# Kernel tuning notes

Measured on AMD Instinct MI355X. Metric: run time of the kernel, lower is better.

The kernel has to match this reference:

```python
import jax, jax.numpy as jnp
import numpy as np

MARGIN = 0.3
EPS = 1e-8  # torch CosineSimilarity eps

N, D = 16384, 256


def setup_inputs() -> dict:
    key = jax.random.key(0)
    k1, k2 = jax.random.split(key)
    x = jax.random.normal(k1, (N, D), dtype=jnp.float32)
    y = jax.random.normal(k2, (N, D), dtype=jnp.float32)
    return {"x": x, "y": y}


def _cosine_matrix(x, y):
    # torch cosine_similarity: dot / max(|x||y|, eps). Normalize rows with eps clamp.
    xn = x / jnp.maximum(jnp.linalg.norm(x, axis=-1, keepdims=True), EPS)
    yn = y / jnp.maximum(jnp.linalg.norm(y, axis=-1, keepdims=True), EPS)
    return xn @ yn.T  # [N, N]


def _rank(S):
    # S[i, j] = cos(x_i, y_j). Positive pair on diagonal.
    diag = jnp.diagonal(S)                      # [N]
    E = jnp.exp(S)                              # [N, N]
    neg_sum = jnp.sum(E, axis=1) - jnp.exp(diag)  # sum over n != i of exp(cos(x_i, y_n))
    m = jnp.exp(diag - MARGIN)                  # margin only on positive term
    ret = m / (m + neg_sum)
    return -jnp.mean(ret)


def reference(x, y):
    S = _cosine_matrix(x, y)
    # bidirectional: rank(x, y) + rank(y, x); rank(y, x) uses transposed sims
    return _rank(S) + _rank(S.T)
```

## Files before the change

### kernel.cpp

```cpp
#include <hip/hip_runtime.h>

#define N_ROWS 16384
#define DIM 256
#define MARGINF 0.3f
#define CH 1024
#define NT 64
#define LOG2E 1.44269504089f

typedef float f32x4 __attribute__((ext_vector_type(4)));
typedef int i32x4 __attribute__((ext_vector_type(4)));
typedef int i32x8 __attribute__((ext_vector_type(8)));

__device__ __forceinline__ float fexp2(float x) {
#if __has_builtin(__builtin_amdgcn_exp2f)
  return __builtin_amdgcn_exp2f(x);
#else
  return exp2f(x);
#endif
}

__device__ __forceinline__ unsigned char to_e4m3(float f) {
  unsigned u = __float_as_uint(f);
  unsigned sign = (u >> 24) & 0x80u;
  float a = fabsf(f);
  if (a >= 448.0f) return (unsigned char)(sign | 0x7eu);
  if (a < 0.015625f) {
    int q = (int)(a * 512.0f + 0.5f);
    return (unsigned char)(sign | (unsigned)q);
  }
  int e;
  float m = frexpf(a, &e);
  float mant = 2.0f * m;
  int e8 = e - 1;
  int mb = (int)(mant * 8.0f + 0.5f) - 8;
  if (mb == 8) { mb = 0; ++e8; if (e8 > 8) return (unsigned char)(sign | 0x7eu); }
  return (unsigned char)(sign | (unsigned)((e8 + 7) << 3) | (unsigned)mb);
}

__device__ __forceinline__ unsigned int pack4_e4m3(float a, float b, float c, float d) {
#if __has_builtin(__builtin_amdgcn_cvt_pk_fp8_f32)
  int lo = __builtin_amdgcn_cvt_pk_fp8_f32(a, b, 0, false);
  int r = __builtin_amdgcn_cvt_pk_fp8_f32(c, d, lo, true);
  return (unsigned int)r;
#else
  return (unsigned int)to_e4m3(a) | ((unsigned int)to_e4m3(b) << 8) |
         ((unsigned int)to_e4m3(c) << 16) | ((unsigned int)to_e4m3(d) << 24);
#endif
}

__global__ __launch_bounds__(256) void normalize_kernel(
    const float* __restrict__ x, const float* __restrict__ y,
    unsigned int* __restrict__ xn8, unsigned int* __restrict__ yn8,
    float* __restrict__ diagF) {
  const int wid = threadIdx.x >> 6;
  const int lane = threadIdx.x & 63;
  const int r = blockIdx.x * 4 + wid;
  const float4 vx = *reinterpret_cast<const float4*>(x + (size_t)r * DIM + lane * 4);
  const float4 vy = *reinterpret_cast<const float4*>(y + (size_t)r * DIM + lane * 4);
  float sx = vx.x * vx.x + vx.y * vx.y + vx.z * vx.z + vx.w * vx.w;
  float sy = vy.x * vy.x + vy.y * vy.y + vy.z * vy.z + vy.w * vy.w;
  float sxy = vx.x * vy.x + vx.y * vy.y + vx.z * vy.z + vx.w * vy.w;
  #pragma unroll
  for (int off = 32; off; off >>= 1) {
    sx += __shfl_xor(sx, off);
    sy += __shfl_xor(sy, off);
    sxy += __shfl_xor(sxy, off);
  }
  const float scx = LOG2E / fmaxf(sqrtf(sx), 1e-8f);
  const float scy = 1.0f / fmaxf(sqrtf(sy), 1e-8f);
  if (lane == 0) diagF[r] = sxy * (scx / LOG2E) * scy;
  xn8[(size_t)r * 64 + lane] = pack4_e4m3(vx.x * scx, vx.y * scx, vx.z * scx, vx.w * scx);
  yn8[(size_t)r * 64 + lane] = pack4_e4m3(vy.x * scy, vy.y * scy, vy.z * scy, vy.w * scy);
}

__device__ __forceinline__ void stage_wave(const unsigned char* __restrict__ src,
                                           int colBase16, unsigned char* slab, int lane) {
  #pragma unroll
  for (int it = 0; it < 4; ++it) {
    const int id = it * 64 + lane;
    const int col = id >> 4;
    const int slot = id & 15;
    const unsigned char* gp =
        src + (unsigned)((colBase16 + col) * DIM + ((slot ^ (col & 7)) << 4));
    unsigned char* l = slab + it * 1024;
    __builtin_amdgcn_global_load_lds(
        (const __attribute__((address_space(1))) unsigned int*)gp,
        (__attribute__((address_space(3))) unsigned int*)l, 16, 0, 0);
  }
}

__global__ __launch_bounds__(256, 2) void gemm_exp_kernel(
    const unsigned char* __restrict__ xn8, const unsigned char* __restrict__ yn8,
    float* __restrict__ rowpart, float* __restrict__ colpartW,
    float* __restrict__ rowsumG, float* __restrict__ colsumG, int use_scratch) {
  __shared__ unsigned char lds[4][2][4096];

  const int tid = threadIdx.x;
  const int lane = tid & 63;
  const int wid = tid >> 6;
  const int grp = lane >> 4, li = lane & 15;

  const int bid = blockIdx.x;
  const int xcd = bid & 7;
  const int rest = bid >> 3;
  const int chunk = xcd * 2 + (rest >> 6);
  const int band = ((rest & 63) << 2) + wid;
  const int rowBase = band * 64;
  const int colBase = chunk * CH;

  i32x8 a[4][2];
  #pragma unroll
  for (int m = 0; m < 4; ++m)
    #pragma unroll
    for (int kb = 0; kb < 2; ++kb) {
      const int row = rowBase + m * 16 + li;
      a[m][kb] = *reinterpret_cast<const i32x8*>(
          xn8 + (size_t)row * DIM + kb * 128 + grp * 32);
    }

  float rsum[4][4];
  #pragma unroll
  for (int m = 0; m < 4; ++m)
    #pragma unroll
    for (int j = 0; j < 4; ++j) rsum[m][j] = 0.0f;

  unsigned char* slab0 = &lds[wid][0][0];
  unsigned char* slab1 = &lds[wid][1][0];
  const int sw = li & 7;
  const int g2 = grp * 2;

  stage_wave(yn8, colBase, slab0, lane);
  __builtin_amdgcn_sched_barrier(0);

  for (int t = 0; t < NT; ++t) {
    if (t + 1 < NT)
      stage_wave(yn8, colBase + (t + 1) * 16, (t & 1) ? slab0 : slab1, lane);
    __builtin_amdgcn_sched_barrier(0);
    if (t == 0)          asm volatile("s_waitcnt vmcnt(4)" ::: "memory");
    else if (t + 1 < NT) asm volatile("s_waitcnt vmcnt(5)" ::: "memory");
    else                 asm volatile("s_waitcnt vmcnt(1)" ::: "memory");
    __builtin_amdgcn_sched_barrier(0);

    const unsigned char* Bp = (t & 1) ? slab1 : slab0;
    const unsigned char* colp = Bp + (size_t)li * 256;
    f32x4 acc[4];
    #pragma unroll
    for (int m = 0; m < 4; ++m) acc[m] = (f32x4)(0.0f);

    __builtin_amdgcn_s_setprio(1);
    #pragma unroll
    for (int kb = 0; kb < 2; ++kb) {
      const int s0 = ((kb * 8 + g2) ^ sw) << 4;
      const int s1 = ((kb * 8 + g2 + 1) ^ sw) << 4;
      const i32x4 blo = *reinterpret_cast<const i32x4*>(colp + s0);
      const i32x4 bhi = *reinterpret_cast<const i32x4*>(colp + s1);
      const i32x8 b = __builtin_shufflevector(blo, bhi, 0, 1, 2, 3, 4, 5, 6, 7);
      #pragma unroll
      for (int m = 0; m < 4; ++m)
        acc[m] = __builtin_amdgcn_mfma_scale_f32_16x16x128_f8f6f4(
            a[m][kb], b, acc[m], 0, 0, 0, 127, 0, 127);
    }
    __builtin_amdgcn_s_setprio(0);

    float cs = 0.0f;
    #pragma unroll
    for (int m = 0; m < 4; ++m) {
      #pragma unroll
      for (int j = 0; j < 4; ++j) {
        const float e = fexp2(acc[m][j]);
        rsum[m][j] += e;
        cs += e;
      }
    }
    cs += __shfl_xor(cs, 16);
    cs += __shfl_xor(cs, 32);
    if (grp == 0) {
      const int c = colBase + t * 16 + li;
      if (use_scratch) colpartW[(size_t)band * N_ROWS + c] = cs;
      else atomicAdd(&colsumG[c], cs);
    }
  }

  #pragma unroll
  for (int m = 0; m < 4; ++m) {
    #pragma unroll
    for (int j = 0; j < 4; ++j) {
      float v = rsum[m][j];
      v += __shfl_xor(v, 1); v += __shfl_xor(v, 2);
      v += __shfl_xor(v, 4); v += __shfl_xor(v, 8);
      if (li == 0) {
        const int r = rowBase + m * 16 + grp * 4 + j;
        if (use_scratch) rowpart[(size_t)chunk * N_ROWS + r] = v;
        else atomicAdd(&rowsumG[r], v);
      }
    }
  }
}

__global__ __launch_bounds__(256) void finalize_kernel(
    const float* __restrict__ rowpart, const float* __restrict__ colpartW,
    const float* __restrict__ rowsumG, const float* __restrict__ colsumG,
    const float* __restrict__ diagF, float* __restrict__ out, int use_scratch) {
  __shared__ float red[4];
  const int i = blockIdx.x * 256 + threadIdx.x;
  float rs, cs;
  if (use_scratch) {
    rs = 0.0f;
    #pragma unroll
    for (int c = 0; c < 16; ++c) rs += rowpart[(size_t)c * N_ROWS + i];
    cs = 0.0f;
    #pragma unroll 8
    for (int b = 0; b < 256; ++b) cs += colpartW[(size_t)b * N_ROWS + i];
  } else {
    rs = rowsumG[i];
    cs = colsumG[i];
  }
  const float d = diagF[i];
  const float e8 = fexp2(LOG2E * d);
  const float mm = __expf(d - MARGINF);
  float v = mm / (mm + rs - e8) + mm / (mm + cs - e8);
  #pragma unroll
  for (int off = 32; off; off >>= 1) v += __shfl_xor(v, off);
  if ((threadIdx.x & 63) == 0) red[threadIdx.x >> 6] = v;
  __syncthreads();
  if (threadIdx.x == 0) {
    const float t = red[0] + red[1] + red[2] + red[3];
    atomicAdd(out, -t / (float)N_ROWS);
  }
}

extern "C" void kernel_launch(void* const* d_in, const int* in_sizes, int n_in,
                              void* d_out, int out_size, void* d_ws, size_t ws_size,
                              hipStream_t stream) {
  const float* x = (const float*)d_in[0];
  const float* y = (const float*)d_in[1];
  char* ws = (char*)d_ws;
  unsigned char* xn8 = (unsigned char*)ws;
  unsigned char* yn8 = (unsigned char*)(ws + (4u << 20));
  float* diagF    = (float*)(ws + (8u << 20));
  float* rowpart  = (float*)(ws + (8u << 20) + 65536);
  float* colpartW = (float*)(ws + (8u << 20) + 65536 + (1u << 20));
  float* rowsumG = rowpart;
  float* colsumG = rowpart + N_ROWS;
  const size_t need_scratch = (8u << 20) + 65536 + (1u << 20) + (16u << 20);
  const int use_scratch = (ws_size >= need_scratch) ? 1 : 0;

  hipMemsetAsync(d_out, 0, sizeof(float), stream);
  if (!use_scratch) hipMemsetAsync(rowsumG, 0, 2 * N_ROWS * sizeof(float), stream);
  normalize_kernel<<<4096, 256, 0, stream>>>(x, y, (unsigned int*)xn8,
                                             (unsigned int*)yn8, diagF);
  gemm_exp_kernel<<<1024, 256, 0, stream>>>(xn8, yn8, rowpart, colpartW,
                                            rowsumG, colsumG, use_scratch);
  finalize_kernel<<<64, 256, 0, stream>>>(rowpart, colpartW, rowsumG, colsumG,
                                          diagF, (float*)d_out, use_scratch);
}
```

Baseline: 118.9 us.

## Pre-swizzle Y into MFMA fragment layout and load B directly from global

The normalize kernel now writes the fp8 Y operand in a layout that matches the per-lane MFMA B fragment, so each wave reads its 32-byte fragments straight from global memory. This removes the LDS staging, the global_load_lds double buffering and the manual vmcnt waits. LDS use is gone, so launch bounds are raised to allow 4 blocks per CU. The cost is that loads are no longer prefetched ahead of use, so latency hiding now depends on occupancy and L2 hits.

```diff
diff --git a/kernel.cpp b/kernel.cpp
--- a/kernel.cpp
+++ b/kernel.cpp
@@ -8,7 +8,6 @@
 #define LOG2E 1.44269504089f
 
 typedef float f32x4 __attribute__((ext_vector_type(4)));
-typedef int i32x4 __attribute__((ext_vector_type(4)));
 typedef int i32x8 __attribute__((ext_vector_type(8)));
 
 __device__ __forceinline__ float fexp2(float x) {
@@ -50,7 +49,7 @@
 
 __global__ __launch_bounds__(256) void normalize_kernel(
     const float* __restrict__ x, const float* __restrict__ y,
-    unsigned int* __restrict__ xn8, unsigned int* __restrict__ yn8,
+    unsigned int* __restrict__ xn8, unsigned char* __restrict__ ybf,
     float* __restrict__ diagF) {
   const int wid = threadIdx.x >> 6;
   const int lane = threadIdx.x & 63;
@@ -70,31 +69,17 @@
   const float scy = 1.0f / fmaxf(sqrtf(sy), 1e-8f);
   if (lane == 0) diagF[r] = sxy * (scx / LOG2E) * scy;
   xn8[(size_t)r * 64 + lane] = pack4_e4m3(vx.x * scx, vx.y * scx, vx.z * scx, vx.w * scx);
-  yn8[(size_t)r * 64 + lane] = pack4_e4m3(vy.x * scy, vy.y * scy, vy.z * scy, vy.w * scy);
-}
-
-__device__ __forceinline__ void stage_wave(const unsigned char* __restrict__ src,
-                                           int colBase16, unsigned char* slab, int lane) {
-  #pragma unroll
-  for (int it = 0; it < 4; ++it) {
-    const int id = it * 64 + lane;
-    const int col = id >> 4;
-    const int slot = id & 15;
-    const unsigned char* gp =
-        src + (unsigned)((colBase16 + col) * DIM + ((slot ^ (col & 7)) << 4));
-    unsigned char* l = slab + it * 1024;
-    __builtin_amdgcn_global_load_lds(
-        (const __attribute__((address_space(1))) unsigned int*)gp,
-        (__attribute__((address_space(3))) unsigned int*)l, 16, 0, 0);
-  }
-}
-
-__global__ __launch_bounds__(256, 2) void gemm_exp_kernel(
-    const unsigned char* __restrict__ xn8, const unsigned char* __restrict__ yn8,
+  const unsigned int py = pack4_e4m3(vy.x * scy, vy.y * scy, vy.z * scy, vy.w * scy);
+  const int t2 = (r >> 4) * 2 + (lane >> 5);
+  const int fl = ((lane >> 3) & 3) * 16 + (r & 15);
+  const unsigned dst = (unsigned)t2 * 2048 + (unsigned)fl * 32 + (lane & 7) * 4;
+  *reinterpret_cast<unsigned int*>(ybf + dst) = py;
+}
+
+__global__ __launch_bounds__(256, 4) void gemm_exp_kernel(
+    const unsigned char* __restrict__ xn8, const unsigned char* __restrict__ ybf,
     float* __restrict__ rowpart, float* __restrict__ colpartW,
     float* __restrict__ rowsumG, float* __restrict__ colsumG, int use_scratch) {
-  __shared__ unsigned char lds[4][2][4096];
-
   const int tid = threadIdx.x;
   const int lane = tid & 63;
   const int wid = tid >> 6;
@@ -124,42 +109,24 @@
     #pragma unroll
     for (int j = 0; j < 4; ++j) rsum[m][j] = 0.0f;
 
-  unsigned char* slab0 = &lds[wid][0][0];
-  unsigned char* slab1 = &lds[wid][1][0];
-  const int sw = li & 7;
-  const int g2 = grp * 2;
-
-  stage_wave(yn8, colBase, slab0, lane);
-  __builtin_amdgcn_sched_barrier(0);
+  const f32x4 z4 = (f32x4)(0.0f);
+  const unsigned char* yb = ybf + (size_t)chunk * (NT * 4096) + (size_t)lane * 32;
 
   for (int t = 0; t < NT; ++t) {
-    if (t + 1 < NT)
-      stage_wave(yn8, colBase + (t + 1) * 16, (t & 1) ? slab0 : slab1, lane);
-    __builtin_amdgcn_sched_barrier(0);
-    if (t == 0)          asm volatile("s_waitcnt vmcnt(4)" ::: "memory");
-    else if (t + 1 < NT) asm volatile("s_waitcnt vmcnt(5)" ::: "memory");
-    else                 asm volatile("s_waitcnt vmcnt(1)" ::: "memory");
-    __builtin_amdgcn_sched_barrier(0);
-
-    const unsigned char* Bp = (t & 1) ? slab1 : slab0;
-    const unsigned char* colp = Bp + (size_t)li * 256;
+    const i32x8 b0 = *reinterpret_cast<const i32x8*>(yb);
+    const i32x8 b1 = *reinterpret_cast<const i32x8*>(yb + 2048);
+    yb += 4096;
+
     f32x4 acc[4];
-    #pragma unroll
-    for (int m = 0; m < 4; ++m) acc[m] = (f32x4)(0.0f);
-
     __builtin_amdgcn_s_setprio(1);
     #pragma unroll
-    for (int kb = 0; kb < 2; ++kb) {
-      const int s0 = ((kb * 8 + g2) ^ sw) << 4;
-      const int s1 = ((kb * 8 + g2 + 1) ^ sw) << 4;
-      const i32x4 blo = *reinterpret_cast<const i32x4*>(colp + s0);
-      const i32x4 bhi = *reinterpret_cast<const i32x4*>(colp + s1);
-      const i32x8 b = __builtin_shufflevector(blo, bhi, 0, 1, 2, 3, 4, 5, 6, 7);
-      #pragma unroll
-      for (int m = 0; m < 4; ++m)
-        acc[m] = __builtin_amdgcn_mfma_scale_f32_16x16x128_f8f6f4(
-            a[m][kb], b, acc[m], 0, 0, 0, 127, 0, 127);
-    }
+    for (int m = 0; m < 4; ++m)
+      acc[m] = __builtin_amdgcn_mfma_scale_f32_16x16x128_f8f6f4(
+          a[m][0], b0, z4, 0, 0, 0, 127, 0, 127);
+    #pragma unroll
+    for (int m = 0; m < 4; ++m)
+      acc[m] = __builtin_amdgcn_mfma_scale_f32_16x16x128_f8f6f4(
+          a[m][1], b1, acc[m], 0, 0, 0, 127, 0, 127);
     __builtin_amdgcn_s_setprio(0);
 
     float cs = 0.0f;
@@ -236,7 +203,7 @@
   const float* y = (const float*)d_in[1];
   char* ws = (char*)d_ws;
   unsigned char* xn8 = (unsigned char*)ws;
-  unsigned char* yn8 = (unsigned char*)(ws + (4u << 20));
+  unsigned char* ybf = (unsigned char*)(ws + (4u << 20));
   float* diagF    = (float*)(ws + (8u << 20));
   float* rowpart  = (float*)(ws + (8u << 20) + 65536);
   float* colpartW = (float*)(ws + (8u << 20) + 65536 + (1u << 20));
@@ -247,9 +214,8 @@
 
   hipMemsetAsync(d_out, 0, sizeof(float), stream);
   if (!use_scratch) hipMemsetAsync(rowsumG, 0, 2 * N_ROWS * sizeof(float), stream);
-  normalize_kernel<<<4096, 256, 0, stream>>>(x, y, (unsigned int*)xn8,
-                                             (unsigned int*)yn8, diagF);
-  gemm_exp_kernel<<<1024, 256, 0, stream>>>(xn8, yn8, rowpart, colpartW,
+  normalize_kernel<<<4096, 256, 0, stream>>>(x, y, (unsigned int*)xn8, ybf, diagF);
+  gemm_exp_kernel<<<1024, 256, 0, stream>>>(xn8, ybf, rowpart, colpartW,
                                             rowsumG, colsumG, use_scratch);
   finalize_kernel<<<64, 256, 0, stream>>>(rowpart, colpartW, rowsumG, colsumG,
                                           diagF, (float*)d_out, use_scratch);
```

After: 105.0 us. -11.7%, faster.
